# Optimization experiments

Measured on AMD Instinct MI355X. Metric: run time of the kernel, lower is better.

The kernel has to match this reference:

```python
import jax, jax.numpy as jnp
import numpy as np

N_NODE = 50000
D_FEAT = 128
N_EDGE = 625000
SIM_THRESH = 0.1


def setup_inputs() -> dict:
    key = jax.random.key(0)
    k1, k2, k3, k4, k5 = jax.random.split(key, 5)
    features = jax.random.normal(k1, (N_NODE, D_FEAT), dtype=jnp.float32)
    edge_weight = jax.random.uniform(k2, (N_EDGE,), dtype=jnp.float32)
    gate = jax.random.uniform(k3, (1,), dtype=jnp.float32)
    row = jax.random.randint(k4, (N_EDGE,), 0, N_NODE)
    col = jax.random.randint(k5, (N_EDGE,), 0, N_NODE)
    # avoid self-loops so the original's att[0,0]==0 / diagonal-removal branches
    # behave as the common (no self-loop) path
    col = jnp.where(col == row, (col + 1) % N_NODE, col)
    edge_index = jnp.stack([row, col], axis=0).astype(jnp.int64)
    return {"edge_index": edge_index, "edge_weight": edge_weight,
            "features": features, "gate": gate}


def reference(edge_index, edge_weight, features, gate):
    n_node = features.shape[0]
    row, col = edge_index[0], edge_index[1]
    # per-edge cosine similarity via normalized feature gather
    nrm = jnp.maximum(jnp.linalg.norm(features, axis=1, keepdims=True), 1e-12)
    fn = features / nrm
    sim = jnp.sum(fn[row] * fn[col], axis=1)            # [E]
    sim = jnp.where(sim < SIM_THRESH, 0.0, sim)         # threshold (all remaining >= 0.1)
    # row-wise L1 normalize over the sparse adjacency
    row_sum = jax.ops.segment_sum(jnp.abs(sim), row, num_segments=n_node)  # [N]
    denom = jnp.where(row_sum > 0, row_sum, 1.0)
    sim_norm = sim / denom[row]
    # degree-based self-loop weight lam = 1/(deg+1); only affects diagonal edges
    degree = jax.ops.segment_sum((sim_norm != 0).astype(sim_norm.dtype), row,
                                 num_segments=n_node)
    lam = 1.0 / (degree + 1.0)
    att_edge = sim_norm + jnp.where(row == col, lam[row], 0.0)
    att_edge = jnp.exp(att_edge)
    # learnable gate blend + clamp
    out = gate[0] * edge_weight + (1.0 - gate[0]) * att_edge
    return jnp.maximum(out, 0.0)
```

## Files before the change

kernel.cpp:

```cpp
#include <hip/hip_runtime.h>
#include <hip/hip_fp16.h>
#include <math.h>

#define N_NODE 50000
#define D_FEAT 128
#define N_EDGE 625000
#define SIM_THRESH 0.1f
#define SCREEN_LO 0.07f
#define BAND_EPS 5e-4f

typedef float v2f __attribute__((ext_vector_type(2)));

__global__ void prep_kernel(const float* __restrict__ feat,
                            float* __restrict__ inv_nrm,
                            __half* __restrict__ fn16,
                            unsigned int* __restrict__ fp8tab,
                            float* __restrict__ row_sum,
                            float* __restrict__ degree) {
    int g = blockIdx.x * blockDim.x + threadIdx.x;
    if (g < N_NODE) { row_sum[g] = 0.0f; degree[g] = 0.0f; }
    int node = g >> 5;
    int lane = g & 31;
    if (node >= N_NODE) return;
    float4 v = ((const float4*)(feat + (size_t)node * D_FEAT))[lane];
    float ss = v.x * v.x + v.y * v.y + v.z * v.z + v.w * v.w;
#pragma unroll
    for (int o = 16; o > 0; o >>= 1) ss += __shfl_down(ss, o, 32);
    ss = __shfl(ss, 0, 32);
    float inv = 1.0f / fmaxf(sqrtf(ss), 1e-12f);
    if (lane == 0) inv_nrm[node] = inv;
    float x0 = v.x * inv, x1 = v.y * inv, x2 = v.z * inv, x3 = v.w * inv;
    __half2 h0 = __floats2half2_rn(x0, x1);
    __half2 h1 = __floats2half2_rn(x2, x3);
    uint2 p;
    p.x = *(unsigned int*)&h0;
    p.y = *(unsigned int*)&h1;
    ((uint2*)(fn16 + (size_t)node * D_FEAT))[lane] = p;
    int w = __builtin_amdgcn_cvt_pk_fp8_f32(x0, x1, 0, false);
    w = __builtin_amdgcn_cvt_pk_fp8_f32(x2, x3, w, true);
    fp8tab[(size_t)node * 32 + lane] = (unsigned int)w;
}

__global__ void edge_sim8_kernel(const int* __restrict__ row,
                                 const int* __restrict__ col,
                                 const float* __restrict__ feat,
                                 const float* __restrict__ inv_nrm,
                                 const __half* __restrict__ fn16,
                                 const unsigned int* __restrict__ fp8tab,
                                 float* __restrict__ sim_out,
                                 float* __restrict__ row_sum,
                                 float* __restrict__ degree) {
    int g = blockIdx.x * blockDim.x + threadIdx.x;
    int edge = g >> 4;
    int lane = g & 15;
    if (edge >= N_EDGE) return;
    int r = row[edge];
    int c = col[edge];

    uint2 aw = ((const uint2*)(fp8tab + (size_t)r * 32))[lane];
    uint2 bw = ((const uint2*)(fp8tab + (size_t)c * 32))[lane];
    v2f a01 = __builtin_amdgcn_cvt_pk_f32_fp8((int)aw.x, false);
    v2f a23 = __builtin_amdgcn_cvt_pk_f32_fp8((int)aw.x, true);
    v2f a45 = __builtin_amdgcn_cvt_pk_f32_fp8((int)aw.y, false);
    v2f a67 = __builtin_amdgcn_cvt_pk_f32_fp8((int)aw.y, true);
    v2f b01 = __builtin_amdgcn_cvt_pk_f32_fp8((int)bw.x, false);
    v2f b23 = __builtin_amdgcn_cvt_pk_f32_fp8((int)bw.x, true);
    v2f b45 = __builtin_amdgcn_cvt_pk_f32_fp8((int)bw.y, false);
    v2f b67 = __builtin_amdgcn_cvt_pk_f32_fp8((int)bw.y, true);
    float d = 0.0f;
    d = fmaf(a01.x, b01.x, d); d = fmaf(a01.y, b01.y, d);
    d = fmaf(a23.x, b23.x, d); d = fmaf(a23.y, b23.y, d);
    d = fmaf(a45.x, b45.x, d); d = fmaf(a45.y, b45.y, d);
    d = fmaf(a67.x, b67.x, d); d = fmaf(a67.y, b67.y, d);
#pragma unroll
    for (int o = 8; o > 0; o >>= 1) d += __shfl_down(d, o, 16);
    d = __shfl(d, 0, 16);

    float s = 0.0f;
    if (d > SCREEN_LO) {
        float4 a = ((const float4*)(fn16 + (size_t)r * D_FEAT))[lane];
        float4 b = ((const float4*)(fn16 + (size_t)c * D_FEAT))[lane];
        const __half2* ah = (const __half2*)&a;
        const __half2* bh = (const __half2*)&b;
        float dh = 0.0f;
#pragma unroll
        for (int i = 0; i < 4; i++) {
            float2 af = __half22float2(ah[i]);
            float2 bf = __half22float2(bh[i]);
            dh = fmaf(af.x, bf.x, dh);
            dh = fmaf(af.y, bf.y, dh);
        }
#pragma unroll
        for (int o = 8; o > 0; o >>= 1) dh += __shfl_down(dh, o, 16);
        dh = __shfl(dh, 0, 16);
        if (fabsf(dh - SIM_THRESH) < BAND_EPS) {
            const float4* fr = (const float4*)(feat + (size_t)r * D_FEAT);
            const float4* fc = (const float4*)(feat + (size_t)c * D_FEAT);
            float4 a0 = fr[lane], a1 = fr[lane + 16];
            float4 b0 = fc[lane], b1 = fc[lane + 16];
            float dd = a0.x * b0.x + a0.y * b0.y + a0.z * b0.z + a0.w * b0.w
                     + a1.x * b1.x + a1.y * b1.y + a1.z * b1.z + a1.w * b1.w;
#pragma unroll
            for (int o = 8; o > 0; o >>= 1) dd += __shfl_down(dd, o, 16);
            dd = __shfl(dd, 0, 16);
            dh = dd * inv_nrm[r] * inv_nrm[c];
        }
        s = (dh < SIM_THRESH) ? 0.0f : dh;
    }
    if (lane == 0) {
        sim_out[edge] = s;
        if (s != 0.0f) {
            atomicAdd(&row_sum[r], s);
            atomicAdd(&degree[r], 1.0f);
        }
    }
}

__global__ void edge_out_kernel(const int* __restrict__ row,
                                const int* __restrict__ col,
                                const float* __restrict__ sim,
                                const float* __restrict__ row_sum,
                                const float* __restrict__ degree,
                                const float* __restrict__ ew,
                                const float* __restrict__ gate,
                                float* __restrict__ out) {
    int e = blockIdx.x * blockDim.x + threadIdx.x;
    if (e >= N_EDGE) return;
    int r = row[e];
    float rs = row_sum[r];
    float denom = (rs > 0.0f) ? rs : 1.0f;
    float att = sim[e] / denom;
    if (r == col[e]) att += 1.0f / (degree[r] + 1.0f);
    att = expf(att);
    float gv = gate[0];
    float o = gv * ew[e] + (1.0f - gv) * att;
    out[e] = fmaxf(o, 0.0f);
}

__global__ void inv_norm_kernel(const float* __restrict__ feat,
                                float* __restrict__ inv_nrm,
                                float* __restrict__ row_sum,
                                float* __restrict__ degree) {
    int g = blockIdx.x * blockDim.x + threadIdx.x;
    if (g < N_NODE) { row_sum[g] = 0.0f; degree[g] = 0.0f; }
    int node = g >> 5;
    int lane = g & 31;
    if (node >= N_NODE) return;
    float4 v = ((const float4*)(feat + (size_t)node * D_FEAT))[lane];
    float ss = v.x * v.x + v.y * v.y + v.z * v.z + v.w * v.w;
#pragma unroll
    for (int o = 16; o > 0; o >>= 1) ss += __shfl_down(ss, o, 32);
    if (lane == 0) inv_nrm[node] = 1.0f / fmaxf(sqrtf(ss), 1e-12f);
}

__global__ void edge_sim_kernel(const int* __restrict__ row,
                                const int* __restrict__ col,
                                const float* __restrict__ feat,
                                const float* __restrict__ inv_nrm,
                                float* __restrict__ sim_out,
                                float* __restrict__ row_sum,
                                float* __restrict__ degree) {
    int g = blockIdx.x * blockDim.x + threadIdx.x;
    int edge = g >> 5;
    int lane = g & 31;
    if (edge >= N_EDGE) return;
    int r = row[edge];
    int c = col[edge];
    float4 a = ((const float4*)(feat + (size_t)r * D_FEAT))[lane];
    float4 b = ((const float4*)(feat + (size_t)c * D_FEAT))[lane];
    float d = a.x * b.x + a.y * b.y + a.z * b.z + a.w * b.w;
#pragma unroll
    for (int o = 16; o > 0; o >>= 1) d += __shfl_down(d, o, 32);
    if (lane == 0) {
        float s = d * inv_nrm[r] * inv_nrm[c];
        if (s < SIM_THRESH) s = 0.0f;
        sim_out[edge] = s;
        if (s != 0.0f) {
            atomicAdd(&row_sum[r], s);
            atomicAdd(&degree[r], 1.0f);
        }
    }
}

extern "C" void kernel_launch(void* const* d_in, const int* in_sizes, int n_in,
                              void* d_out, int out_size, void* d_ws, size_t ws_size,
                              hipStream_t stream) {
    const int*   edge_index = (const int*)d_in[0];
    const float* ew         = (const float*)d_in[1];
    const float* feat       = (const float*)d_in[2];
    const float* gate       = (const float*)d_in[3];
    float*       out        = (float*)d_out;

    const int* row = edge_index;
    const int* col = edge_index + N_EDGE;

    float* row_sum = (float*)d_ws;
    float* degree  = row_sum + N_NODE;
    float* inv_nrm = degree + N_NODE;
    float* sim     = inv_nrm + N_NODE;
    __half* fn16   = (__half*)(sim + N_EDGE);
    unsigned int* fp8tab = (unsigned int*)(fn16 + (size_t)N_NODE * D_FEAT);

    size_t need = (size_t)(3 * N_NODE + N_EDGE) * 4
                + (size_t)N_NODE * D_FEAT * 2
                + (size_t)N_NODE * D_FEAT;

    const int block = 256;

    if (ws_size >= need) {
        {
            long long threads = (long long)N_NODE * 32;
            prep_kernel<<<(int)((threads + block - 1) / block), block, 0, stream>>>(
                feat, inv_nrm, fn16, fp8tab, row_sum, degree);
        }
        {
            long long threads = (long long)N_EDGE * 16;
            edge_sim8_kernel<<<(int)((threads + block - 1) / block), block, 0, stream>>>(
                row, col, feat, inv_nrm, fn16, fp8tab, sim, row_sum, degree);
        }
        edge_out_kernel<<<(N_EDGE + block - 1) / block, block, 0, stream>>>(
            row, col, sim, row_sum, degree, ew, gate, out);
    } else {
        {
            long long threads = (long long)N_NODE * 32;
            inv_norm_kernel<<<(int)((threads + block - 1) / block), block, 0, stream>>>(
                feat, inv_nrm, row_sum, degree);
        }
        {
            long long threads = (long long)N_EDGE * 32;
            edge_sim_kernel<<<(int)((threads + block - 1) / block), block, 0, stream>>>(
                row, col, feat, inv_nrm, sim, row_sum, degree);
        }
        edge_out_kernel<<<(N_EDGE + block - 1) / block, block, 0, stream>>>(
            row, col, sim, row_sum, degree, ew, gate, out);
    }
}
```

Before: 134.6 us.

## Bucket edges by row (CSR) and compute per-row similarity without atomics

Builds a CSR-like grouping of edges by source row (count, single-block scan, atomic scatter), then processes each row with a 16-lane group. The row's fp16 features stay in registers and the row sum and degree are reduced locally, with sims buffered in shared memory, so the float atomics and the separate output kernel are gone. The cost is extra launches, a serial single-block scan, a scatter with atomics, and random-order writes to out. Row degrees vary, so per-group work is unbalanced and high-degree rows spill their sims to global memory.

```diff
diff --git a/kernel.cpp b/kernel.cpp
--- a/kernel.cpp
+++ b/kernel.cpp
@@ -8,8 +8,184 @@
 #define SIM_THRESH 0.1f
 #define SCREEN_LO 0.07f
 #define BAND_EPS 5e-4f
+#define MAXDEG 128
 
 typedef float v2f __attribute__((ext_vector_type(2)));
+
+
+__global__ void prep_count_kernel(const float* __restrict__ feat,
+                                  const int* __restrict__ row,
+                                  float* __restrict__ inv_nrm,
+                                  __half* __restrict__ fn16,
+                                  unsigned int* __restrict__ fp8tab,
+                                  unsigned int* __restrict__ bcnt) {
+    int g = blockIdx.x * blockDim.x + threadIdx.x;
+    if (g < N_EDGE) atomicAdd(&bcnt[row[g]], 1u);
+    int node = g >> 5;
+    int lane = g & 31;
+    if (node >= N_NODE) return;
+    float4 v = ((const float4*)(feat + (size_t)node * D_FEAT))[lane];
+    float ss = v.x * v.x + v.y * v.y + v.z * v.z + v.w * v.w;
+#pragma unroll
+    for (int o = 16; o > 0; o >>= 1) ss += __shfl_down(ss, o, 32);
+    ss = __shfl(ss, 0, 32);
+    float inv = 1.0f / fmaxf(sqrtf(ss), 1e-12f);
+    if (lane == 0) inv_nrm[node] = inv;
+    float x0 = v.x * inv, x1 = v.y * inv, x2 = v.z * inv, x3 = v.w * inv;
+    __half2 h0 = __floats2half2_rn(x0, x1);
+    __half2 h1 = __floats2half2_rn(x2, x3);
+    uint2 p;
+    p.x = *(unsigned int*)&h0;
+    p.y = *(unsigned int*)&h1;
+    ((uint2*)(fn16 + (size_t)node * D_FEAT))[lane] = p;
+    int w = __builtin_amdgcn_cvt_pk_fp8_f32(x0, x1, 0, false);
+    w = __builtin_amdgcn_cvt_pk_fp8_f32(x2, x3, w, true);
+    fp8tab[(size_t)node * 32 + lane] = (unsigned int)w;
+}
+
+__global__ __launch_bounds__(1024)
+void scan_kernel(const unsigned int* __restrict__ cnt,
+                 unsigned int* __restrict__ bstart,
+                 unsigned int* __restrict__ cursor) {
+    __shared__ unsigned int ls[1024];
+    const int CH = (N_NODE + 1023) / 1024;
+    int t = threadIdx.x;
+    int base = t * CH;
+    unsigned int s = 0;
+    for (int i = 0; i < CH; i++) {
+        int idx = base + i;
+        if (idx < N_NODE) s += cnt[idx];
+    }
+    ls[t] = s;
+    __syncthreads();
+    for (int off = 1; off < 1024; off <<= 1) {
+        unsigned int v = (t >= off) ? ls[t - off] : 0u;
+        __syncthreads();
+        ls[t] += v;
+        __syncthreads();
+    }
+    unsigned int run = (t == 0) ? 0u : ls[t - 1];
+    for (int i = 0; i < CH; i++) {
+        int idx = base + i;
+        if (idx <= N_NODE) {
+            bstart[idx] = run;
+            if (idx < N_NODE) { cursor[idx] = run; run += cnt[idx]; }
+        }
+    }
+}
+
+__global__ void scatter_kernel(const int* __restrict__ row,
+                               const int* __restrict__ col,
+                               unsigned int* __restrict__ cursor,
+                               uint2* __restrict__ pairs) {
+    int e = blockIdx.x * blockDim.x + threadIdx.x;
+    if (e >= N_EDGE) return;
+    int r = row[e];
+    unsigned int pos = atomicAdd(&cursor[r], 1u);
+    uint2 pr;
+    pr.x = (unsigned int)col[e];
+    pr.y = (unsigned int)e;
+    pairs[pos] = pr;
+}
+
+__global__ __launch_bounds__(256)
+void row_sim_kernel(const uint2* __restrict__ pairs,
+                    const unsigned int* __restrict__ bstart,
+                    const float* __restrict__ feat,
+                    const float* __restrict__ inv_nrm,
+                    const __half* __restrict__ fn16,
+                    const unsigned int* __restrict__ fp8tab,
+                    const float* __restrict__ ew,
+                    const float* __restrict__ gate,
+                    float* __restrict__ simspill,
+                    float* __restrict__ out) {
+    __shared__ float simbuf[16][MAXDEG];
+    int g = blockIdx.x * 16 + (threadIdx.x >> 4);
+    int lane = threadIdx.x & 15;
+    int lg = threadIdx.x >> 4;
+    if (g >= N_NODE) return;
+    unsigned int s0 = bstart[g], s1 = bstart[g + 1];
+    if (s0 == s1) return;
+
+    float4 a = ((const float4*)(fn16 + (size_t)g * D_FEAT))[lane];
+    const __half2* ah = (const __half2*)&a;
+    float2 af[4];
+#pragma unroll
+    for (int i = 0; i < 4; i++) af[i] = __half22float2(ah[i]);
+
+    float row_sum = 0.0f, deg = 0.0f;
+
+    for (unsigned int p = s0; p < s1; p++) {
+        uint2 pr = pairs[p];
+        int c = (int)pr.x;
+        uint2 bw = ((const uint2*)(fp8tab + (size_t)c * 32))[lane];
+        v2f b01 = __builtin_amdgcn_cvt_pk_f32_fp8((int)bw.x, false);
+        v2f b23 = __builtin_amdgcn_cvt_pk_f32_fp8((int)bw.x, true);
+        v2f b45 = __builtin_amdgcn_cvt_pk_f32_fp8((int)bw.y, false);
+        v2f b67 = __builtin_amdgcn_cvt_pk_f32_fp8((int)bw.y, true);
+        float d = 0.0f;
+        d = fmaf(af[0].x, b01.x, d); d = fmaf(af[0].y, b01.y, d);
+        d = fmaf(af[1].x, b23.x, d); d = fmaf(af[1].y, b23.y, d);
+        d = fmaf(af[2].x, b45.x, d); d = fmaf(af[2].y, b45.y, d);
+        d = fmaf(af[3].x, b67.x, d); d = fmaf(af[3].y, b67.y, d);
+#pragma unroll
+        for (int o = 8; o > 0; o >>= 1) d += __shfl_down(d, o, 16);
+        d = __shfl(d, 0, 16);
+
+        float s = 0.0f;
+        if (d > SCREEN_LO) {
+            float4 b = ((const float4*)(fn16 + (size_t)c * D_FEAT))[lane];
+            const __half2* bh = (const __half2*)&b;
+            float dh = 0.0f;
+#pragma unroll
+            for (int i = 0; i < 4; i++) {
+                float2 bf = __half22float2(bh[i]);
+                dh = fmaf(af[i].x, bf.x, dh);
+                dh = fmaf(af[i].y, bf.y, dh);
+            }
+#pragma unroll
+            for (int o = 8; o > 0; o >>= 1) dh += __shfl_down(dh, o, 16);
+            dh = __shfl(dh, 0, 16);
+            if (fabsf(dh - SIM_THRESH) < BAND_EPS) {
+                const float4* fr = (const float4*)(feat + (size_t)g * D_FEAT);
+                const float4* fc = (const float4*)(feat + (size_t)c * D_FEAT);
+                float4 a0 = fr[lane], a1 = fr[lane + 16];
+                float4 b0 = fc[lane], b1 = fc[lane + 16];
+                float dd = a0.x * b0.x + a0.y * b0.y + a0.z * b0.z + a0.w * b0.w
+                         + a1.x * b1.x + a1.y * b1.y + a1.z * b1.z + a1.w * b1.w;
+#pragma unroll
+                for (int o = 8; o > 0; o >>= 1) dd += __shfl_down(dd, o, 16);
+                dd = __shfl(dd, 0, 16);
+                dh = dd * inv_nrm[g] * inv_nrm[c];
+            }
+            s = (dh < SIM_THRESH) ? 0.0f : dh;
+        }
+        row_sum += s;
+        deg += (s != 0.0f) ? 1.0f : 0.0f;
+        unsigned int k = p - s0;
+        if (lane == 0) {
+            if (k < MAXDEG) simbuf[lg][k] = s;
+            else simspill[p] = s;
+        }
+    }
+
+    float denom = (row_sum > 0.0f) ? row_sum : 1.0f;
+    float lam = 1.0f / (deg + 1.0f);
+    float gv = gate[0];
+
+    for (unsigned int p = s0 + lane; p < s1; p += 16) {
+        uint2 pr = pairs[p];
+        int c = (int)pr.x;
+        unsigned int orig = pr.y;
+        unsigned int k = p - s0;
+        float s = (k < MAXDEG) ? simbuf[lg][k] : simspill[p];
+        float att = s / denom;
+        if (c == g) att += lam;
+        att = expf(att);
+        float o = gv * ew[orig] + (1.0f - gv) * att;
+        out[orig] = fmaxf(o, 0.0f);
+    }
+}
 
 __global__ void prep_kernel(const float* __restrict__ feat,
                             float* __restrict__ inv_nrm,
@@ -56,7 +232,6 @@
     if (edge >= N_EDGE) return;
     int r = row[edge];
     int c = col[edge];
-
     uint2 aw = ((const uint2*)(fp8tab + (size_t)r * 32))[lane];
     uint2 bw = ((const uint2*)(fp8tab + (size_t)c * 32))[lane];
     v2f a01 = __builtin_amdgcn_cvt_pk_f32_fp8((int)aw.x, false);
@@ -75,7 +250,6 @@
 #pragma unroll
     for (int o = 8; o > 0; o >>= 1) d += __shfl_down(d, o, 16);
     d = __shfl(d, 0, 16);
-
     float s = 0.0f;
     if (d > SCREEN_LO) {
         float4 a = ((const float4*)(fn16 + (size_t)r * D_FEAT))[lane];
@@ -85,10 +259,10 @@
         float dh = 0.0f;
 #pragma unroll
         for (int i = 0; i < 4; i++) {
-            float2 af = __half22float2(ah[i]);
-            float2 bf = __half22float2(bh[i]);
-            dh = fmaf(af.x, bf.x, dh);
-            dh = fmaf(af.y, bf.y, dh);
+            float2 afv = __half22float2(ah[i]);
+            float2 bfv = __half22float2(bh[i]);
+            dh = fmaf(afv.x, bfv.x, dh);
+            dh = fmaf(afv.y, bfv.y, dh);
         }
 #pragma unroll
         for (int o = 8; o > 0; o >>= 1) dh += __shfl_down(dh, o, 16);
@@ -137,51 +311,6 @@
     out[e] = fmaxf(o, 0.0f);
 }
 
-__global__ void inv_norm_kernel(const float* __restrict__ feat,
-                                float* __restrict__ inv_nrm,
-                                float* __restrict__ row_sum,
-                                float* __restrict__ degree) {
-    int g = blockIdx.x * blockDim.x + threadIdx.x;
-    if (g < N_NODE) { row_sum[g] = 0.0f; degree[g] = 0.0f; }
-    int node = g >> 5;
-    int lane = g & 31;
-    if (node >= N_NODE) return;
-    float4 v = ((const float4*)(feat + (size_t)node * D_FEAT))[lane];
-    float ss = v.x * v.x + v.y * v.y + v.z * v.z + v.w * v.w;
-#pragma unroll
-    for (int o = 16; o > 0; o >>= 1) ss += __shfl_down(ss, o, 32);
-    if (lane == 0) inv_nrm[node] = 1.0f / fmaxf(sqrtf(ss), 1e-12f);
-}
-
-__global__ void edge_sim_kernel(const int* __restrict__ row,
-                                const int* __restrict__ col,
-                                const float* __restrict__ feat,
-                                const float* __restrict__ inv_nrm,
-                                float* __restrict__ sim_out,
-                                float* __restrict__ row_sum,
-                                float* __restrict__ degree) {
-    int g = blockIdx.x * blockDim.x + threadIdx.x;
-    int edge = g >> 5;
-    int lane = g & 31;
-    if (edge >= N_EDGE) return;
-    int r = row[edge];
-    int c = col[edge];
-    float4 a = ((const float4*)(feat + (size_t)r * D_FEAT))[lane];
-    float4 b = ((const float4*)(feat + (size_t)c * D_FEAT))[lane];
-    float d = a.x * b.x + a.y * b.y + a.z * b.z + a.w * b.w;
-#pragma unroll
-    for (int o = 16; o > 0; o >>= 1) d += __shfl_down(d, o, 32);
-    if (lane == 0) {
-        float s = d * inv_nrm[r] * inv_nrm[c];
-        if (s < SIM_THRESH) s = 0.0f;
-        sim_out[edge] = s;
-        if (s != 0.0f) {
-            atomicAdd(&row_sum[r], s);
-            atomicAdd(&degree[r], 1.0f);
-        }
-    }
-}
-
 extern "C" void kernel_launch(void* const* d_in, const int* in_sizes, int n_in,
                               void* d_out, int out_size, void* d_ws, size_t ws_size,
                               hipStream_t stream) {
@@ -194,44 +323,55 @@
     const int* row = edge_index;
     const int* col = edge_index + N_EDGE;
 
+    const int block = 256;
+
+    char* base = (char*)d_ws;
+    size_t off = 0;
+    uint2* pairs = (uint2*)(base + off);           off += (size_t)N_EDGE * 8;
+    __half* fn16 = (__half*)(base + off);          off += (size_t)N_NODE * D_FEAT * 2;
+    unsigned int* fp8tab = (unsigned int*)(base + off); off += (size_t)N_NODE * D_FEAT;
+    float* inv_nrm = (float*)(base + off);         off += (size_t)N_NODE * 4;
+    unsigned int* bstart = (unsigned int*)(base + off); off += (size_t)(N_NODE + 1) * 4;
+    unsigned int* cursor = (unsigned int*)(base + off); off += (size_t)N_NODE * 4;
+    unsigned int* bcnt = (unsigned int*)(base + off);   off += (size_t)N_NODE * 4;
+    float* simspill = (float*)(base + off);        off += (size_t)N_EDGE * 4;
+    size_t need_fast = off;
+
+    if (ws_size >= need_fast) {
+        hipMemsetAsync(bcnt, 0, (size_t)N_NODE * 4, stream);
+        {
+            long long threads = (long long)N_NODE * 32;
+            prep_count_kernel<<<(int)((threads + block - 1) / block), block, 0, stream>>>(
+                feat, row, inv_nrm, fn16, fp8tab, bcnt);
+        }
+        scan_kernel<<<1, 1024, 0, stream>>>(bcnt, bstart, cursor);
+        scatter_kernel<<<(N_EDGE + block - 1) / block, block, 0, stream>>>(
+            row, col, cursor, pairs);
+        {
+            int blocks = (N_NODE + 15) / 16;
+            row_sim_kernel<<<blocks, block, 0, stream>>>(
+                pairs, bstart, feat, inv_nrm, fn16, fp8tab, ew, gate,
+                simspill, out);
+        }
+        return;
+    }
+
     float* row_sum = (float*)d_ws;
     float* degree  = row_sum + N_NODE;
-    float* inv_nrm = degree + N_NODE;
-    float* sim     = inv_nrm + N_NODE;
-    __half* fn16   = (__half*)(sim + N_EDGE);
-    unsigned int* fp8tab = (unsigned int*)(fn16 + (size_t)N_NODE * D_FEAT);
-
-    size_t need = (size_t)(3 * N_NODE + N_EDGE) * 4
-                + (size_t)N_NODE * D_FEAT * 2
-                + (size_t)N_NODE * D_FEAT;
-
-    const int block = 256;
-
-    if (ws_size >= need) {
-        {
-            long long threads = (long long)N_NODE * 32;
-            prep_kernel<<<(int)((threads + block - 1) / block), block, 0, stream>>>(
-                feat, inv_nrm, fn16, fp8tab, row_sum, degree);
-        }
-        {
-            long long threads = (long long)N_EDGE * 16;
-            edge_sim8_kernel<<<(int)((threads + block - 1) / block), block, 0, stream>>>(
-                row, col, feat, inv_nrm, fn16, fp8tab, sim, row_sum, degree);
-        }
-        edge_out_kernel<<<(N_EDGE + block - 1) / block, block, 0, stream>>>(
-            row, col, sim, row_sum, degree, ew, gate, out);
-    } else {
-        {
-            long long threads = (long long)N_NODE * 32;
-            inv_norm_kernel<<<(int)((threads + block - 1) / block), block, 0, stream>>>(
-                feat, inv_nrm, row_sum, degree);
-        }
-        {
-            long long threads = (long long)N_EDGE * 32;
-            edge_sim_kernel<<<(int)((threads + block - 1) / block), block, 0, stream>>>(
-                row, col, feat, inv_nrm, sim, row_sum, degree);
-        }
-        edge_out_kernel<<<(N_EDGE + block - 1) / block, block, 0, stream>>>(
-            row, col, sim, row_sum, degree, ew, gate, out);
-    }
-}
+    float* inv_nrm2 = degree + N_NODE;
+    float* sim     = inv_nrm2 + N_NODE;
+    __half* fn16b  = (__half*)(sim + N_EDGE);
+    unsigned int* fp8tabb = (unsigned int*)(fn16b + (size_t)N_NODE * D_FEAT);
+    {
+        long long threads = (long long)N_NODE * 32;
+        prep_kernel<<<(int)((threads + block - 1) / block), block, 0, stream>>>(
+            feat, inv_nrm2, fn16b, fp8tabb, row_sum, degree);
+    }
+    {
+        long long threads = (long long)N_EDGE * 16;
+        edge_sim8_kernel<<<(int)((threads + block - 1) / block), block, 0, stream>>>(
+            row, col, feat, inv_nrm2, fn16b, fp8tabb, sim, row_sum, degree);
+    }
+    edge_out_kernel<<<(N_EDGE + block - 1) / block, block, 0, stream>>>(
+        row, col, sim, row_sum, degree, ew, gate, out);
+}
```

Result: slower. 326.3 us (+142.5%).

## Partition edge similarity work by column-node slice to improve cache locality

Applied to the files above, without the earlier changes.

Each 64-edge chunk is now handled by eight blocks, one per slice of column-node ids. A block only processes the edges whose column falls in its slice, so the column-feature gathers from blocks that run at the same time fall in a smaller range of nodes and may hit in cache more often. The cost is that every block reads col for all 64 edges and skips most of them, so lanes sit idle through divergence. The grid also becomes eight times larger, adding launch and scheduling overhead.

```diff
diff --git a/kernel.cpp b/kernel.cpp
--- a/kernel.cpp
+++ b/kernel.cpp
@@ -8,6 +8,9 @@
 #define SIM_THRESH 0.1f
 #define SCREEN_LO 0.07f
 #define BAND_EPS 5e-4f
+
+#define N_SLICE 8
+#define SLICE_DIV 6250
 
 typedef float v2f __attribute__((ext_vector_type(2)));
 
@@ -41,77 +44,85 @@
     fp8tab[(size_t)node * 32 + lane] = (unsigned int)w;
 }
 
-__global__ void edge_sim8_kernel(const int* __restrict__ row,
-                                 const int* __restrict__ col,
-                                 const float* __restrict__ feat,
-                                 const float* __restrict__ inv_nrm,
-                                 const __half* __restrict__ fn16,
-                                 const unsigned int* __restrict__ fp8tab,
-                                 float* __restrict__ sim_out,
-                                 float* __restrict__ row_sum,
-                                 float* __restrict__ degree) {
-    int g = blockIdx.x * blockDim.x + threadIdx.x;
-    int edge = g >> 4;
-    int lane = g & 15;
-    if (edge >= N_EDGE) return;
-    int r = row[edge];
-    int c = col[edge];
-
-    uint2 aw = ((const uint2*)(fp8tab + (size_t)r * 32))[lane];
-    uint2 bw = ((const uint2*)(fp8tab + (size_t)c * 32))[lane];
-    v2f a01 = __builtin_amdgcn_cvt_pk_f32_fp8((int)aw.x, false);
-    v2f a23 = __builtin_amdgcn_cvt_pk_f32_fp8((int)aw.x, true);
-    v2f a45 = __builtin_amdgcn_cvt_pk_f32_fp8((int)aw.y, false);
-    v2f a67 = __builtin_amdgcn_cvt_pk_f32_fp8((int)aw.y, true);
-    v2f b01 = __builtin_amdgcn_cvt_pk_f32_fp8((int)bw.x, false);
-    v2f b23 = __builtin_amdgcn_cvt_pk_f32_fp8((int)bw.x, true);
-    v2f b45 = __builtin_amdgcn_cvt_pk_f32_fp8((int)bw.y, false);
-    v2f b67 = __builtin_amdgcn_cvt_pk_f32_fp8((int)bw.y, true);
-    float d = 0.0f;
-    d = fmaf(a01.x, b01.x, d); d = fmaf(a01.y, b01.y, d);
-    d = fmaf(a23.x, b23.x, d); d = fmaf(a23.y, b23.y, d);
-    d = fmaf(a45.x, b45.x, d); d = fmaf(a45.y, b45.y, d);
-    d = fmaf(a67.x, b67.x, d); d = fmaf(a67.y, b67.y, d);
-#pragma unroll
-    for (int o = 8; o > 0; o >>= 1) d += __shfl_down(d, o, 16);
-    d = __shfl(d, 0, 16);
-
-    float s = 0.0f;
-    if (d > SCREEN_LO) {
-        float4 a = ((const float4*)(fn16 + (size_t)r * D_FEAT))[lane];
-        float4 b = ((const float4*)(fn16 + (size_t)c * D_FEAT))[lane];
-        const __half2* ah = (const __half2*)&a;
-        const __half2* bh = (const __half2*)&b;
-        float dh = 0.0f;
-#pragma unroll
-        for (int i = 0; i < 4; i++) {
-            float2 af = __half22float2(ah[i]);
-            float2 bf = __half22float2(bh[i]);
-            dh = fmaf(af.x, bf.x, dh);
-            dh = fmaf(af.y, bf.y, dh);
-        }
-#pragma unroll
-        for (int o = 8; o > 0; o >>= 1) dh += __shfl_down(dh, o, 16);
-        dh = __shfl(dh, 0, 16);
-        if (fabsf(dh - SIM_THRESH) < BAND_EPS) {
-            const float4* fr = (const float4*)(feat + (size_t)r * D_FEAT);
-            const float4* fc = (const float4*)(feat + (size_t)c * D_FEAT);
-            float4 a0 = fr[lane], a1 = fr[lane + 16];
-            float4 b0 = fc[lane], b1 = fc[lane + 16];
-            float dd = a0.x * b0.x + a0.y * b0.y + a0.z * b0.z + a0.w * b0.w
-                     + a1.x * b1.x + a1.y * b1.y + a1.z * b1.z + a1.w * b1.w;
-#pragma unroll
-            for (int o = 8; o > 0; o >>= 1) dd += __shfl_down(dd, o, 16);
-            dd = __shfl(dd, 0, 16);
-            dh = dd * inv_nrm[r] * inv_nrm[c];
-        }
-        s = (dh < SIM_THRESH) ? 0.0f : dh;
-    }
-    if (lane == 0) {
-        sim_out[edge] = s;
-        if (s != 0.0f) {
-            atomicAdd(&row_sum[r], s);
-            atomicAdd(&degree[r], 1.0f);
+__global__ __launch_bounds__(256)
+void edge_sim8_sliced_kernel(const int* __restrict__ row,
+                             const int* __restrict__ col,
+                             const float* __restrict__ feat,
+                             const float* __restrict__ inv_nrm,
+                             const __half* __restrict__ fn16,
+                             const unsigned int* __restrict__ fp8tab,
+                             float* __restrict__ sim_out,
+                             float* __restrict__ row_sum,
+                             float* __restrict__ degree) {
+    int slice = blockIdx.x & (N_SLICE - 1);
+    int chunk = blockIdx.x >> 3;
+    int grp  = threadIdx.x >> 4;
+    int lane = threadIdx.x & 15;
+
+#pragma unroll
+    for (int n = 0; n < 4; n++) {
+        int e = chunk * 64 + n * 16 + grp;
+        if (e >= N_EDGE) break;
+        int c = col[e];
+        if ((unsigned)c / SLICE_DIV != (unsigned)slice) continue;
+        int r = row[e];
+
+        uint2 aw = ((const uint2*)(fp8tab + (size_t)r * 32))[lane];
+        uint2 bw = ((const uint2*)(fp8tab + (size_t)c * 32))[lane];
+        v2f a01 = __builtin_amdgcn_cvt_pk_f32_fp8((int)aw.x, false);
+        v2f a23 = __builtin_amdgcn_cvt_pk_f32_fp8((int)aw.x, true);
+        v2f a45 = __builtin_amdgcn_cvt_pk_f32_fp8((int)aw.y, false);
+        v2f a67 = __builtin_amdgcn_cvt_pk_f32_fp8((int)aw.y, true);
+        v2f b01 = __builtin_amdgcn_cvt_pk_f32_fp8((int)bw.x, false);
+        v2f b23 = __builtin_amdgcn_cvt_pk_f32_fp8((int)bw.x, true);
+        v2f b45 = __builtin_amdgcn_cvt_pk_f32_fp8((int)bw.y, false);
+        v2f b67 = __builtin_amdgcn_cvt_pk_f32_fp8((int)bw.y, true);
+        float d = 0.0f;
+        d = fmaf(a01.x, b01.x, d); d = fmaf(a01.y, b01.y, d);
+        d = fmaf(a23.x, b23.x, d); d = fmaf(a23.y, b23.y, d);
+        d = fmaf(a45.x, b45.x, d); d = fmaf(a45.y, b45.y, d);
+        d = fmaf(a67.x, b67.x, d); d = fmaf(a67.y, b67.y, d);
+#pragma unroll
+        for (int o = 8; o > 0; o >>= 1) d += __shfl_down(d, o, 16);
+        d = __shfl(d, 0, 16);
+
+        float s = 0.0f;
+        if (d > SCREEN_LO) {
+            float4 a = ((const float4*)(fn16 + (size_t)r * D_FEAT))[lane];
+            float4 b = ((const float4*)(fn16 + (size_t)c * D_FEAT))[lane];
+            const __half2* ah = (const __half2*)&a;
+            const __half2* bh = (const __half2*)&b;
+            float dh = 0.0f;
+#pragma unroll
+            for (int i = 0; i < 4; i++) {
+                float2 afv = __half22float2(ah[i]);
+                float2 bfv = __half22float2(bh[i]);
+                dh = fmaf(afv.x, bfv.x, dh);
+                dh = fmaf(afv.y, bfv.y, dh);
+            }
+#pragma unroll
+            for (int o = 8; o > 0; o >>= 1) dh += __shfl_down(dh, o, 16);
+            dh = __shfl(dh, 0, 16);
+            if (fabsf(dh - SIM_THRESH) < BAND_EPS) {
+                const float4* fr = (const float4*)(feat + (size_t)r * D_FEAT);
+                const float4* fc = (const float4*)(feat + (size_t)c * D_FEAT);
+                float4 a0 = fr[lane], a1 = fr[lane + 16];
+                float4 b0 = fc[lane], b1 = fc[lane + 16];
+                float dd = a0.x * b0.x + a0.y * b0.y + a0.z * b0.z + a0.w * b0.w
+                         + a1.x * b1.x + a1.y * b1.y + a1.z * b1.z + a1.w * b1.w;
+#pragma unroll
+                for (int o = 8; o > 0; o >>= 1) dd += __shfl_down(dd, o, 16);
+                dd = __shfl(dd, 0, 16);
+                dh = dd * inv_nrm[r] * inv_nrm[c];
+            }
+            s = (dh < SIM_THRESH) ? 0.0f : dh;
+        }
+        if (lane == 0) {
+            sim_out[e] = s;
+            if (s != 0.0f) {
+                atomicAdd(&row_sum[r], s);
+                atomicAdd(&degree[r], 1.0f);
+            }
         }
     }
 }
@@ -214,8 +225,9 @@
                 feat, inv_nrm, fn16, fp8tab, row_sum, degree);
         }
         {
-            long long threads = (long long)N_EDGE * 16;
-            edge_sim8_kernel<<<(int)((threads + block - 1) / block), block, 0, stream>>>(
+            int chunks = (N_EDGE + 63) / 64;
+            int blocks = chunks * N_SLICE;
+            edge_sim8_sliced_kernel<<<blocks, block, 0, stream>>>(
                 row, col, feat, inv_nrm, fn16, fp8tab, sim, row_sum, degree);
         }
         edge_out_kernel<<<(N_EDGE + block - 1) / block, block, 0, stream>>>(
```

Result: slower. 237.9 us (+76.8%).
